# Kernel tuning notes

Measured on AMD Instinct MI355X. Metric: run time of the kernel, lower is better.

The kernel has to match this reference:

```python
import jax, jax.numpy as jnp
import numpy as np

GRID_SIZE = 5
SPLINE_ORDER = 3
GRID_RANGE = (-1.0, 1.0)
KERNEL = 3
N_CONVS = 8


def make_grid():
    # Matches KANLinear: arange(-K, G+K+1) * h + grid_range[0]
    h = (GRID_RANGE[1] - GRID_RANGE[0]) / GRID_SIZE
    return jnp.arange(-SPLINE_ORDER, GRID_SIZE + SPLINE_ORDER + 1, dtype=jnp.float32) * h + GRID_RANGE[0]


def b_splines(x, grid):
    # x: (..., kk) -> bases: (..., kk, grid_size + spline_order)
    x = x[..., None]
    bases = ((x >= grid[:-1]) & (x < grid[1:])).astype(x.dtype)
    for p in range(1, SPLINE_ORDER + 1):
        left = (x - grid[: -(p + 1)]) / (grid[p:-1] - grid[: -(p + 1)])
        right = (grid[p + 1:] - x) / (grid[p + 1:] - grid[1:-p])
        bases = left * bases[..., :-1] + right * bases[..., 1:]
    return bases


def setup_inputs() -> dict:
    key = jax.random.key(0)
    k1, k2, k3, k4 = jax.random.split(key, 4)
    B, C, H, W = 16, 32, 64, 64
    kk = KERNEL * KERNEL
    S = GRID_SIZE + SPLINE_ORDER  # number of spline coefficients per input
    x = jax.random.normal(k1, (B, C, H, W), jnp.float32)
    base_w = jax.random.normal(k2, (N_CONVS, kk), jnp.float32) * (1.0 / np.sqrt(kk))
    spline_w = jax.random.normal(k3, (N_CONVS, kk, S), jnp.float32) * 0.1
    spline_scaler = jax.random.normal(k4, (N_CONVS, kk), jnp.float32) * (1.0 / np.sqrt(kk))
    return {"x": x, "base_w": base_w, "spline_w": spline_w, "spline_scaler": spline_scaler}


def reference(x, base_w, spline_w, spline_scaler):
    B, C, H, W = x.shape
    kk = KERNEL * KERNEL
    Ho, Wo = H - KERNEL + 1, W - KERNEL + 1  # stride 1, no pad, no dilation
    # im2col: (B, C*kk, Ho, Wo), feature dim ordered (C, kh, kw) like torch Unfold
    patches = jax.lax.conv_general_dilated_patches(x, (KERNEL, KERNEL), (1, 1), "VALID")
    patches = patches.reshape(B, C, kk, Ho * Wo).transpose(0, 1, 3, 2)  # (B,C,L,kk)
    grid = make_grid()
    basis = b_splines(patches, grid)  # (B,C,L,kk,S)
    scaled_w = spline_w * spline_scaler[..., None]  # (n_convs, kk, S)
    base_out = jnp.einsum("bclk,nk->bcnl", jax.nn.silu(patches), base_w)
    spline_out = jnp.einsum("bclks,nks->bcnl", basis, scaled_w)
    # output channel layout: channel*n_convs + kern
    out = (base_out + spline_out).reshape(B, C * N_CONVS, Ho, Wo)
    return out
```

## Files before the change

### kernel.cpp

```cpp
#include <hip/hip_runtime.h>


constexpr int Hh = 64, Ww = 64;
constexpr int Ho = 62, Wo = 62;
constexpr int L  = Ho * Wo;
constexpr int NC = 8;
constexpr int RW  = 5;
constexpr int RPB = 20;
constexpr int SR  = RPB + 2;
constexpr int NPX = SR * Ww;
constexpr int NSTRIP = 4;

__global__ __launch_bounds__(128)
void fold_weights(const float* __restrict__ bw, const float* __restrict__ sw,
                  const float* __restrict__ scl, float* __restrict__ wf)
{
    int i = threadIdx.x;
    if (i < 72) {
        const int n = i & 7;
        const int k = i >> 3;
        const int m = n * 9 + k;
        const float sc = scl[m];
        wf[k * 72 + 0 * 8 + n] = bw[m];
#pragma unroll
        for (int f = 1; f < 9; f++)
            wf[k * 72 + f * 8 + n] = sw[m * 8 + (f - 1)] * sc;
    }
}

__global__ __launch_bounds__(256, 3)
void kan_conv_kernel(const float* __restrict__ x,
                     const float* __restrict__ wf,
                     float* __restrict__ out)
{
    __shared__ float  ssh[NPX];
    __shared__ float4 bsh0[NPX];
    __shared__ float4 bsh1[NPX];

    const int strip = blockIdx.x & (NSTRIP - 1);
    const int bc    = blockIdx.x >> 2;
    const int s0    = strip * RPB;

    const int stage_rows = (s0 + SR <= Hh) ? SR : (Hh - s0);
    const int npx = stage_rows * Ww;
    const float* xp = x + (size_t)bc * (Hh * Ww) + (size_t)s0 * Ww;

    for (int p = threadIdx.x; p < npx; p += 256) {
        const float v  = xp[p];
        ssh[p] = v / (1.0f + __expf(-v));

        const float u  = (v + 2.2f) * 2.5f;
        const float fj = floorf(u);
        const float t  = u - fj;
        const int   j  = (int)fj - 3;
        const float om = 1.0f - t;
        const float t2 = t * t;
        const float w3 = t * t2 * (1.0f / 6.0f);
        const float w0 = om * om * om * (1.0f / 6.0f);
        const float w1 = fmaf(t2, fmaf(t, 0.5f, -1.0f), 2.0f / 3.0f);
        const float w2 = 1.0f - w0 - w1 - w3;

        float b[8];
#pragma unroll
        for (int s = 0; s < 8; s++) {
            float r = 0.0f;
            r = (j == s    ) ? w0 : r;
            r = (j == s - 1) ? w1 : r;
            r = (j == s - 2) ? w2 : r;
            r = (j == s - 3) ? w3 : r;
            b[s] = r;
        }
        bsh0[p] = make_float4(b[0], b[1], b[2], b[3]);
        bsh1[p] = make_float4(b[4], b[5], b[6], b[7]);
    }
    __syncthreads();

    const int wv = threadIdx.x >> 6;
    const int ln = threadIdx.x & 63;
    const int rbase = wv * RW;

    if (ln < Wo && s0 + rbase < Ho) {
        float acc[RW][NC];
#pragma unroll
        for (int r = 0; r < RW; r++)
#pragma unroll
            for (int n = 0; n < NC; n++) acc[r][n] = 0.0f;

#pragma unroll 1
        for (int k = 0; k < 9; k++) {
            const int kh = k / 3;
            const int kw = k - kh * 3;
            const float* __restrict__ w = wf + k * 72;

#pragma unroll
            for (int r = 0; r < RW; r++) {
                const int px = (rbase + r + kh) * Ww + ln + kw;
                const float  f0 = ssh[px];
                const float4 ba = bsh0[px];
                const float4 bb = bsh1[px];
#pragma unroll
                for (int n = 0; n < NC; n++) {
                    float a = acc[r][n];
                    a = fmaf(f0,   w[     n], a);
                    a = fmaf(ba.x, w[ 8 + n], a);
                    a = fmaf(ba.y, w[16 + n], a);
                    a = fmaf(ba.z, w[24 + n], a);
                    a = fmaf(ba.w, w[32 + n], a);
                    a = fmaf(bb.x, w[40 + n], a);
                    a = fmaf(bb.y, w[48 + n], a);
                    a = fmaf(bb.z, w[56 + n], a);
                    a = fmaf(bb.w, w[64 + n], a);
                    acc[r][n] = a;
                }
            }
        }

#pragma unroll
        for (int r = 0; r < RW; r++) {
            const int orow = s0 + rbase + r;
            if (orow < Ho) {
                const size_t ob = (size_t)bc * NC * L + (size_t)orow * Wo + ln;
#pragma unroll
                for (int n = 0; n < NC; n++) out[ob + (size_t)n * L] = acc[r][n];
            }
        }
    }
}

extern "C" void kernel_launch(void* const* d_in, const int* in_sizes, int n_in,
                              void* d_out, int out_size, void* d_ws, size_t ws_size,
                              hipStream_t stream) {
    const float* x   = (const float*)d_in[0];
    const float* bw  = (const float*)d_in[1];
    const float* sw  = (const float*)d_in[2];
    const float* scl = (const float*)d_in[3];
    float* wf  = (float*)d_ws;
    float* out = (float*)d_out;

    fold_weights<<<1, 128, 0, stream>>>(bw, sw, scl, wf);

    const int planes = in_sizes[0] / (Hh * Ww);
    dim3 grid(planes * NSTRIP);
    kan_conv_kernel<<<grid, 256, 0, stream>>>(x, wf, out);
}
```

Measured before the change: 113.6 us.

## Compute KAN conv contraction with bf16 MFMA instead of scalar FMAs

The per-pixel 9-tap by 9-feature by 8-conv contraction now runs on MFMA 16x16x32 bf16 instructions instead of scalar FP32 FMAs. Features (silu plus 8 spline bases) are packed as bf16 into a swizzled LDS layout, and weights are prepacked as bf16 MFMA A-fragments. Row strips shrink to 12 rows across 6 strips and occupancy rises to 4 blocks. Rounding weights and bases to bf16 costs accuracy, and the output stores from the MFMA accumulator layout may be less coalesced.

```diff
diff --git a/kernel.cpp b/kernel.cpp
--- a/kernel.cpp
+++ b/kernel.cpp
@@ -1,45 +1,59 @@
 #include <hip/hip_runtime.h>
 
+
+typedef __attribute__((ext_vector_type(8))) short bf16x8;
+typedef __attribute__((ext_vector_type(4))) float f32x4;
 
 constexpr int Hh = 64, Ww = 64;
 constexpr int Ho = 62, Wo = 62;
 constexpr int L  = Ho * Wo;
 constexpr int NC = 8;
-constexpr int RW  = 5;
-constexpr int RPB = 20;
+constexpr int RPB = 12;
 constexpr int SR  = RPB + 2;
+constexpr int NSTRIP = 6;
 constexpr int NPX = SR * Ww;
-constexpr int NSTRIP = 4;
+constexpr int LDS_PX = NPX + 4;
+constexpr int ZQ = LDS_PX * 2;
 
-__global__ __launch_bounds__(128)
+__global__ __launch_bounds__(64)
 void fold_weights(const float* __restrict__ bw, const float* __restrict__ sw,
-                  const float* __restrict__ scl, float* __restrict__ wf)
+                  const float* __restrict__ scl, ushort* __restrict__ wf)
 {
-    int i = threadIdx.x;
-    if (i < 72) {
-        const int n = i & 7;
-        const int k = i >> 3;
-        const int m = n * 9 + k;
-        const float sc = scl[m];
-        wf[k * 72 + 0 * 8 + n] = bw[m];
-#pragma unroll
-        for (int f = 1; f < 9; f++)
-            wf[k * 72 + f * 8 + n] = sw[m * 8 + (f - 1)] * sc;
+    const int l = threadIdx.x;
+    const int conv = l & 15;
+    const int g = l >> 4;
+    for (int c = 0; c < 5; c++) {
+        const int tap = 2 * c + (g >> 1);
+        for (int j = 0; j < 8; j++) {
+            const int slot = (g & 1) * 8 + j;
+            float v = 0.0f;
+            if (conv < 8 && tap < 9) {
+                const int m = conv * 9 + tap;
+                if (slot == 0)      v = bw[m];
+                else if (slot <= 8) v = sw[m * 8 + (slot - 1)] * scl[m];
+            }
+            wf[(c * 64 + l) * 8 + j] = (ushort)((__float_as_uint(v) + 0x8000u) >> 16);
+        }
     }
 }
 
-__global__ __launch_bounds__(256, 3)
+__device__ __forceinline__ uint pk(float lo, float hi) {
+    return ((__float_as_uint(lo) + 0x8000u) >> 16) |
+           ((__float_as_uint(hi) + 0x8000u) & 0xffff0000u);
+}
+
+__global__ __launch_bounds__(256, 4)
 void kan_conv_kernel(const float* __restrict__ x,
-                     const float* __restrict__ wf,
+                     const ushort* __restrict__ wf,
                      float* __restrict__ out)
 {
-    __shared__ float  ssh[NPX];
-    __shared__ float4 bsh0[NPX];
-    __shared__ float4 bsh1[NPX];
+    __shared__ uint4 pix[LDS_PX * 2 + 2];
 
-    const int strip = blockIdx.x & (NSTRIP - 1);
-    const int bc    = blockIdx.x >> 2;
+    const int strip = blockIdx.x % NSTRIP;
+    const int bc    = blockIdx.x / NSTRIP;
     const int s0    = strip * RPB;
+
+    if (threadIdx.x < 2) pix[ZQ + threadIdx.x] = make_uint4(0, 0, 0, 0);
 
     const int stage_rows = (s0 + SR <= Hh) ? SR : (Hh - s0);
     const int npx = stage_rows * Ww;
@@ -47,7 +61,7 @@
 
     for (int p = threadIdx.x; p < npx; p += 256) {
         const float v  = xp[p];
-        ssh[p] = v / (1.0f + __expf(-v));
+        const float sv = v / (1.0f + __expf(-v));
 
         const float u  = (v + 2.2f) * 2.5f;
         const float fj = floorf(u);
@@ -70,59 +84,60 @@
             r = (j == s - 3) ? w3 : r;
             b[s] = r;
         }
-        bsh0[p] = make_float4(b[0], b[1], b[2], b[3]);
-        bsh1[p] = make_float4(b[4], b[5], b[6], b[7]);
+
+        const int sw_ = (p >> 2) & 1;
+        pix[p * 2 + sw_]       = make_uint4(pk(sv, b[0]), pk(b[1], b[2]),
+                                            pk(b[3], b[4]), pk(b[5], b[6]));
+        pix[p * 2 + (1 - sw_)] = make_uint4(pk(b[7], 0.0f), 0u, 0u, 0u);
     }
     __syncthreads();
 
     const int wv = threadIdx.x >> 6;
-    const int ln = threadIdx.x & 63;
-    const int rbase = wv * RW;
+    const int l  = threadIdx.x & 63;
+    const int g  = l >> 4;
+    const int m  = l & 15;
+    const int h  = g & 1;
+    const int c0 = wv * 16;
 
-    if (ln < Wo && s0 + rbase < Ho) {
-        float acc[RW][NC];
+    bf16x8 wa[5];
+    const uint4* wfv = (const uint4*)wf;
 #pragma unroll
-        for (int r = 0; r < RW; r++)
+    for (int c = 0; c < 5; c++) {
+        uint4 q = wfv[c * 64 + l];
+        wa[c] = *(const bf16x8*)&q;
+    }
+
+    int dtap[5];
 #pragma unroll
-            for (int n = 0; n < NC; n++) acc[r][n] = 0.0f;
+    for (int c = 0; c < 5; c++) {
+        int tap = 2 * c + (g >> 1);
+        if (tap > 8) tap = 8;
+        dtap[c] = (tap / 3) * Ww + (tap % 3);
+    }
 
-#pragma unroll 1
-        for (int k = 0; k < 9; k++) {
-            const int kh = k / 3;
-            const int kw = k - kh * 3;
-            const float* __restrict__ w = wf + k * 72;
+    const int nrt  = (s0 + RPB <= Ho) ? RPB : (Ho - s0);
+    const int pcol = c0 + m;
+    const char* pixb = (const char*)pix;
 
+    for (int rl = 0; rl < nrt; rl++) {
+        const int ptile = rl * Ww + pcol;
+        f32x4 acc = {0.0f, 0.0f, 0.0f, 0.0f};
 #pragma unroll
-            for (int r = 0; r < RW; r++) {
-                const int px = (rbase + r + kh) * Ww + ln + kw;
-                const float  f0 = ssh[px];
-                const float4 ba = bsh0[px];
-                const float4 bb = bsh1[px];
-#pragma unroll
-                for (int n = 0; n < NC; n++) {
-                    float a = acc[r][n];
-                    a = fmaf(f0,   w[     n], a);
-                    a = fmaf(ba.x, w[ 8 + n], a);
-                    a = fmaf(ba.y, w[16 + n], a);
-                    a = fmaf(ba.z, w[24 + n], a);
-                    a = fmaf(ba.w, w[32 + n], a);
-                    a = fmaf(bb.x, w[40 + n], a);
-                    a = fmaf(bb.y, w[48 + n], a);
-                    a = fmaf(bb.z, w[56 + n], a);
-                    a = fmaf(bb.w, w[64 + n], a);
-                    acc[r][n] = a;
-                }
-            }
+        for (int c = 0; c < 5; c++) {
+            const int p = ptile + dtap[c];
+            int addr = (p << 5) + ((((p >> 2) & 1) ^ h) << 4);
+            if (c == 4 && g >= 2) addr = ZQ * 16;
+            const bf16x8 bfrag = *(const bf16x8*)(pixb + addr);
+            acc = __builtin_amdgcn_mfma_f32_16x16x32_bf16(wa[c], bfrag, acc, 0, 0, 0);
         }
 
-#pragma unroll
-        for (int r = 0; r < RW; r++) {
-            const int orow = s0 + rbase + r;
-            if (orow < Ho) {
-                const size_t ob = (size_t)bc * NC * L + (size_t)orow * Wo + ln;
-#pragma unroll
-                for (int n = 0; n < NC; n++) out[ob + (size_t)n * L] = acc[r][n];
-            }
+        if (g < 2 && pcol < Wo) {
+            float* op = out + ((size_t)bc * NC + g * 4) * L
+                            + (size_t)(s0 + rl) * Wo + pcol;
+            op[0 * L] = acc.x;
+            op[1 * L] = acc.y;
+            op[2 * L] = acc.z;
+            op[3 * L] = acc.w;
         }
     }
 }
@@ -134,10 +149,10 @@
     const float* bw  = (const float*)d_in[1];
     const float* sw  = (const float*)d_in[2];
     const float* scl = (const float*)d_in[3];
-    float* wf  = (float*)d_ws;
+    ushort* wf = (ushort*)d_ws;
     float* out = (float*)d_out;
 
-    fold_weights<<<1, 128, 0, stream>>>(bw, sw, scl, wf);
+    fold_weights<<<1, 64, 0, stream>>>(bw, sw, scl, wf);
 
     const int planes = in_sizes[0] / (Hh * Ww);
     dim3 grid(planes * NSTRIP);
```

Measured after the change: 104.9 us. 1.08x faster.
